# Performance work log

Hardware: AMD Instinct MI355X
Metric: run time of the kernel (lower is better)

The kernel has to match this reference:

```python
import jax, jax.numpy as jnp
import numpy as np

V, D, S, L, H, NC = 32000, 768, 1024, 4, 12, 16
HS = D // H
B = 8

def _layernorm(x, w, b, eps=1e-5):
    mu = jnp.mean(x, axis=-1, keepdims=True)
    var = jnp.mean(jnp.square(x - mu), axis=-1, keepdims=True)
    return (x - mu) * jax.lax.rsqrt(var + eps) * w + b


def setup_inputs() -> dict:
    key = jax.random.key(0)
    ks = jax.random.split(key, 24)
    s = 0.02
    inp = {
        "x": jax.random.randint(ks[0], (B, S), 0, V, dtype=jnp.int64) if jax.config.jax_enable_x64 else jax.random.randint(ks[0], (B, S), 0, V, dtype=jnp.int32),
        "attention_mask": jnp.ones((B, S), dtype=jnp.int32),
        "tok_emb": jax.random.normal(ks[1], (V, D), jnp.float32) * s,
        "pos_emb": jax.random.normal(ks[2], (S, D), jnp.float32) * s,
        "Wq": jax.random.normal(ks[3], (L, H, D, HS), jnp.float32) * s,
        "Wk": jax.random.normal(ks[4], (L, H, D, HS), jnp.float32) * s,
        "Wv": jax.random.normal(ks[5], (L, H, D, HS), jnp.float32) * s,
        "Wo": jax.random.normal(ks[6], (L, D, D), jnp.float32) * s,
        "bo": jnp.zeros((L, D), jnp.float32),
        "ln1_w": jnp.ones((L, D), jnp.float32),
        "ln1_b": jnp.zeros((L, D), jnp.float32),
        "ln2_w": jnp.ones((L, D), jnp.float32),
        "ln2_b": jnp.zeros((L, D), jnp.float32),
        "W1": jax.random.normal(ks[7], (L, D, 4 * D), jnp.float32) * s,
        "b1": jnp.zeros((L, 4 * D), jnp.float32),
        "W2": jax.random.normal(ks[8], (L, 4 * D, D), jnp.float32) * s,
        "b2": jnp.zeros((L, D), jnp.float32),
        "lnf_w": jnp.ones((D,), jnp.float32),
        "lnf_b": jnp.zeros((D,), jnp.float32),
        "cW1": jax.random.normal(ks[9], (D, 4 * D), jnp.float32) * s,
        "cb1": jnp.zeros((4 * D,), jnp.float32),
        "cW2": jax.random.normal(ks[10], (4 * D, NC), jnp.float32) * s,
        "cb2": jnp.zeros((NC,), jnp.float32),
    }
    return inp


def reference(x, attention_mask, tok_emb, pos_emb, Wq, Wk, Wv, Wo, bo,
              ln1_w, ln1_b, ln2_w, ln2_b, W1, b1, W2, b2,
              lnf_w, lnf_b, cW1, cb1, cW2, cb2):
    b, s = x.shape
    h = tok_emb[x] + pos_emb[jnp.arange(s)][None, :, :]  # [B,S,D]
    key_mask = (attention_mask == 0)[:, None, None, :]   # [B,1,1,S] masks keys
    scale = jnp.asarray(D, h.dtype) ** -0.5              # NOTE: scales by embed_dim, as in source
    for l in range(L):
        xn = _layernorm(h, ln1_w[l], ln1_b[l])
        q = jnp.einsum('bsd,hde->bhse', xn, Wq[l])
        k = jnp.einsum('bsd,hde->bhse', xn, Wk[l])
        v = jnp.einsum('bsd,hde->bhse', xn, Wv[l])
        wei = jnp.einsum('bhqe,bhke->bhqk', q, k) * scale
        wei = jnp.where(key_mask, -jnp.inf, wei)
        att = jax.nn.softmax(wei, axis=-1)               # dropout = identity (eval)
        out = jnp.einsum('bhqk,bhke->bhqe', att, v)      # [B,H,S,HS]
        out = out.transpose(0, 2, 1, 3).reshape(b, s, D)  # concat heads
        h = h + out @ Wo[l] + bo[l]
        xn2 = _layernorm(h, ln2_w[l], ln2_b[l])
        h = h + jax.nn.relu(xn2 @ W1[l] + b1[l]) @ W2[l] + b2[l]
    h = _layernorm(h, lnf_w, lnf_b)
    last = h[:, -1, :]                                   # pool=None -> last position
    logits = jax.nn.relu(last @ cW1 + cb1) @ cW2 + cb2
    return logits
```

## Files before the change

kernel.cpp:

```cpp
#include <hip/hip_runtime.h>
#include <hip/hip_bf16.h>

#define D_MODEL 768
#define SEQ     1024
#define NB      8
#define NHEAD   12
#define HS      64
#define NLAYER  4
#define DFF     3072
#define NCLS    16
#define MROWS   (NB*SEQ)

typedef float f32x4  __attribute__((ext_vector_type(4)));
typedef short bf16x8 __attribute__((ext_vector_type(8)));

__device__ __forceinline__ short f2bf_s(float x) {
    __hip_bfloat16 h = __float2bfloat16(x);
    union { __hip_bfloat16 h; short s; } u; u.h = h; return u.s;
}

__device__ __forceinline__ void gld16(const void* g, void* l) {
    __builtin_amdgcn_global_load_lds((const __attribute__((address_space(1))) void*)g,
                                     (__attribute__((address_space(3))) void*)l, 16, 0, 0);
}

__global__ __launch_bounds__(256) void embed_kernel(
    const int* __restrict__ x, const float* __restrict__ tok,
    const float* __restrict__ pos, float* __restrict__ h)
{
    int row = blockIdx.x;
    int s   = row & (SEQ - 1);
    int t   = threadIdx.x;
    int id  = x[row];
    const float* te = tok + (size_t)id * D_MODEL;
    const float* pe = pos + (size_t)s  * D_MODEL;
    float* hr = h + (size_t)row * D_MODEL;
    for (int d = t; d < D_MODEL; d += 256) hr[d] = te[d] + pe[d];
}

template<int BF16OUT>
__global__ __launch_bounds__(256) void ln_kernel(
    const float* __restrict__ in, const float* __restrict__ w,
    const float* __restrict__ b, void* __restrict__ outv,
    int row_stride, int row_offset)
{
    __shared__ float red[256];
    int r = blockIdx.x;
    const float* xr = in + (size_t)(r * row_stride + row_offset) * D_MODEL;
    int t = threadIdx.x;
    float v0 = xr[t], v1 = xr[t + 256], v2 = xr[t + 512];
    red[t] = v0 + v1 + v2; __syncthreads();
    for (int off = 128; off; off >>= 1) { if (t < off) red[t] += red[t + off]; __syncthreads(); }
    float mu = red[0] * (1.f / D_MODEL);
    __syncthreads();
    float d0 = v0 - mu, d1 = v1 - mu, d2 = v2 - mu;
    red[t] = d0*d0 + d1*d1 + d2*d2; __syncthreads();
    for (int off = 128; off; off >>= 1) { if (t < off) red[t] += red[t + off]; __syncthreads(); }
    float rstd = rsqrtf(red[0] * (1.f / D_MODEL) + 1e-5f);
    float y0 = d0 * rstd * w[t]       + b[t];
    float y1 = d1 * rstd * w[t + 256] + b[t + 256];
    float y2 = d2 * rstd * w[t + 512] + b[t + 512];
    if (BF16OUT) {
        __hip_bfloat16* yr = (__hip_bfloat16*)outv + (size_t)r * D_MODEL;
        yr[t] = __float2bfloat16(y0); yr[t+256] = __float2bfloat16(y1); yr[t+512] = __float2bfloat16(y2);
    } else {
        float* yr = (float*)outv + (size_t)r * D_MODEL;
        yr[t] = y0; yr[t+256] = y1; yr[t+512] = y2;
    }
}

template<int MODE>
__global__ __launch_bounds__(256) void convw_kernel(
    const float* __restrict__ W, __hip_bfloat16* __restrict__ BT,
    int K, int N, size_t in_stride, size_t out_stride)
{
    __shared__ __hip_bfloat16 sT[64][72];
    W  += (size_t)blockIdx.z * in_stride;
    BT += (size_t)blockIdx.z * out_stride;
    int k0 = blockIdx.x * 64, n0 = blockIdx.y * 64;
    int t = threadIdx.x;
    int kl = t >> 4, nl4 = (t & 15) * 4;
    #pragma unroll
    for (int i = 0; i < 4; i++) {
        int k = k0 + kl + i * 16;
        int n = n0 + nl4;
        const float* src = (MODE == 0) ? (W + (size_t)k * N + n)
                                       : (W + ((size_t)(n >> 6) * K + k) * 64 + (n & 63));
        float4 v = *(const float4*)src;
        sT[nl4 + 0][kl + i*16] = __float2bfloat16(v.x);
        sT[nl4 + 1][kl + i*16] = __float2bfloat16(v.y);
        sT[nl4 + 2][kl + i*16] = __float2bfloat16(v.z);
        sT[nl4 + 3][kl + i*16] = __float2bfloat16(v.w);
    }
    __syncthreads();
    int nl = t >> 2, seg = (t & 3) * 16;
    uint4* dst = (uint4*)(BT + (size_t)(n0 + nl) * K + k0 + seg);
    dst[0] = *(uint4*)&sT[nl][seg];
    dst[1] = *(uint4*)&sT[nl][seg + 8];
}

template<int OMODE>
__global__ __launch_bounds__(256, 3) void gemm128(
    const __hip_bfloat16* __restrict__ A, const __hip_bfloat16* __restrict__ BT,
    const float* __restrict__ bias, const float* __restrict__ res,
    void* __restrict__ Cv, int M, int N, int K, int relu)
{
    __shared__ short sA[2][128 * 32];
    __shared__ short sB[2][128 * 32];
    int t = threadIdx.x;
    int wave = t >> 6, lane = t & 63;
    int l16 = lane & 15, quad = (lane >> 4) & 3;
    int wm = wave >> 1, wn = wave & 1;
    int bm = blockIdx.x * 128, bn = blockIdx.y * 128;

    int kbeg = 0, kend = K;
    if (OMODE == 3) { int KS = K >> 1; kbeg = blockIdx.z * KS; kend = kbeg + KS; }

    int u = lane >> 2;
    int skey = ((u & 3) ^ ((u >> 2) & 3));
    int sseg = (lane & 3) ^ skey;
    int c0 = wave * 2, c1 = wave * 2 + 1;
    int rA0 = c0 * 16 + u, rA1 = c1 * 16 + u;
    int fkey = ((l16 & 3) ^ ((l16 >> 2) & 3));

    const f32x4 zf = {0.f, 0.f, 0.f, 0.f};
    f32x4 acc[4][4];
    #pragma unroll
    for (int mi = 0; mi < 4; mi++)
        #pragma unroll
        for (int ni = 0; ni < 4; ni++) acc[mi][ni] = zf;

    #define STAGE(bufi, kk) do { \
        gld16(A  + (size_t)(bm + rA0) * K + (kk) + sseg * 8, &sA[bufi][c0 * 512]); \
        gld16(A  + (size_t)(bm + rA1) * K + (kk) + sseg * 8, &sA[bufi][c1 * 512]); \
        gld16(BT + (size_t)(bn + rA0) * K + (kk) + sseg * 8, &sB[bufi][c0 * 512]); \
        gld16(BT + (size_t)(bn + rA1) * K + (kk) + sseg * 8, &sB[bufi][c1 * 512]); \
    } while (0)

    STAGE(0, kbeg);
    __syncthreads();
    int buf = 0;
    for (int k0 = kbeg; k0 < kend; k0 += 32) {
        int kn = k0 + 32;
        if (kn < kend) STAGE(buf ^ 1, kn);
        bf16x8 aF[4], bF[4];
        #pragma unroll
        for (int mi = 0; mi < 4; mi++)
            aF[mi] = *(bf16x8*)&sA[buf][(wm * 64 + mi * 16 + l16) * 32 + ((quad ^ fkey) * 8)];
        #pragma unroll
        for (int ni = 0; ni < 4; ni++)
            bF[ni] = *(bf16x8*)&sB[buf][(wn * 64 + ni * 16 + l16) * 32 + ((quad ^ fkey) * 8)];
        #pragma unroll
        for (int ni = 0; ni < 4; ni++)
            #pragma unroll
            for (int mi = 0; mi < 4; mi++)
                acc[mi][ni] = __builtin_amdgcn_mfma_f32_16x16x32_bf16(aF[mi], bF[ni], acc[mi][ni], 0, 0, 0);
        __syncthreads();
        buf ^= 1;
    }
    #undef STAGE

    #pragma unroll
    for (int mi = 0; mi < 4; mi++) {
        #pragma unroll
        for (int ni = 0; ni < 4; ni++) {
            int row0 = bm + wm * 64 + mi * 16 + quad * 4;
            int col  = bn + wn * 64 + ni * 16 + l16;
            #pragma unroll
            for (int r = 0; r < 4; r++) {
                int row = row0 + r;
                float v = acc[mi][ni][r];
                if (OMODE == 3) {
                    float* C = (float*)Cv;
                    if (blockIdx.z == 0 && bias) v += bias[col];
                    unsafeAtomicAdd(&C[(size_t)row * N + col], v);
                    continue;
                }
                if (OMODE != 1 && bias) v += bias[col];
                if (relu) v = fmaxf(v, 0.f);
                if (OMODE == 0) {
                    float* C = (float*)Cv;
                    if (res) v += res[(size_t)row * N + col];
                    C[(size_t)row * N + col] = v;
                } else if (OMODE == 1) {
                    int which = col / D_MODEL, cc = col % D_MODEL;
                    int bb = row >> 10, ss = row & 1023, hh = cc >> 6, e = cc & 63;
                    ((__hip_bfloat16*)Cv)[(size_t)which * MROWS * D_MODEL +
                        (((size_t)(bb * NHEAD + hh)) * SEQ + ss) * HS + e] = __float2bfloat16(v);
                } else {
                    ((__hip_bfloat16*)Cv)[(size_t)row * N + col] = __float2bfloat16(v);
                }
            }
        }
    }
    (void)M;
}

__global__ __launch_bounds__(256) void vtrans_kernel(
    const __hip_bfloat16* __restrict__ vb, __hip_bfloat16* __restrict__ vt)
{
    __shared__ short tile[64][66];
    int bh = blockIdx.x, st = blockIdx.y;
    const short* src = (const short*)vb + ((size_t)bh * SEQ + st * 64) * HS;
    int t = threadIdx.x;
    #pragma unroll
    for (int i = 0; i < 2; i++) {
        int slot = t + i * 256;
        int row = slot >> 3, seg = slot & 7;
        *(uint4*)&tile[row][seg * 8] = *(const uint4*)(src + row * HS + seg * 8);
    }
    __syncthreads();
    short* dst = (short*)vt + (size_t)bh * HS * SEQ + st * 64;
    #pragma unroll
    for (int i = 0; i < 2; i++) {
        int slot = t + i * 256;
        int e = slot >> 3, seg = slot & 7;
        union { uint4 u; short s[8]; } pk;
        #pragma unroll
        for (int j = 0; j < 8; j++) pk.s[j] = tile[seg * 8 + j][e];
        *(uint4*)(dst + (size_t)e * SEQ + seg * 8) = pk.u;
    }
}

__global__ __launch_bounds__(128, 2) void attn_mfma_kernel(
    const __hip_bfloat16* __restrict__ q, const __hip_bfloat16* __restrict__ k,
    const __hip_bfloat16* __restrict__ v, const int* __restrict__ mask,
    __hip_bfloat16* __restrict__ ao)
{
    __shared__ short sK[2][64 * 64];
    __shared__ short sVT[2][64 * 64];
    __shared__ short sP[2][64 * 64];
    __shared__ float mskf[SEQ];
    int bid = blockIdx.x;
    int xcd = bid & 7, j = bid >> 3;
    int bh  = ((j >> 3) << 3) | xcd;
    int qt8 = j & 7;
    int b = bh / NHEAD, hh = bh % NHEAD;
    int t = threadIdx.x, w = t >> 6, lane = t & 63;
    int l16 = lane & 15, quad = lane >> 4;
    const float scale = 0.036084391824351615f;
    const f32x4 zf = {0.f, 0.f, 0.f, 0.f};

    #pragma unroll
    for (int i = 0; i < 8; i++) {
        int idx = t + i * 128;
        mskf[idx] = mask[b * SEQ + idx] ? 0.f : -1e30f;
    }

    int qb0 = qt8 * 128 + w * 64;
    const __hip_bfloat16* qbase = q + ((size_t)bh * SEQ + qb0) * HS;
    bf16x8 qf[4][2];
    #pragma unroll
    for (int qt = 0; qt < 4; qt++)
        #pragma unroll
        for (int s = 0; s < 2; s++)
            qf[qt][s] = *(const bf16x8*)(qbase + (qt * 16 + l16) * HS + s * 32 + quad * 8);

    f32x4 accO[4][4];
    float m_st[4], l_st[4];
    #pragma unroll
    for (int dt = 0; dt < 4; dt++)
        #pragma unroll
        for (int qt = 0; qt < 4; qt++) accO[dt][qt] = zf;
    #pragma unroll
    for (int qt = 0; qt < 4; qt++) { m_st[qt] = -1e30f; l_st[qt] = 0.f; }

    int rowL = lane >> 3;
    int sgl = ((lane & 7) ^ ((lane >> 3) & 7)) * 8;
    const __hip_bfloat16* kg0 = k + ((size_t)bh * SEQ) * HS;
    const __hip_bfloat16* vtg0 = v + (size_t)bh * HS * SEQ;
    short* myP = &sP[w][0];

    #pragma unroll
    for (int i = 0; i < 4; i++) {
        int c = w * 4 + i;
        int rr = c * 8 + rowL;
        gld16(kg0  + (size_t)rr * HS  + sgl, (char*)&sK[0][0]  + c * 1024);
        gld16(vtg0 + (size_t)rr * SEQ + sgl, (char*)&sVT[0][0] + c * 1024);
    }
    __syncthreads();

    int buf = 0;
    for (int kc = 0; kc < 16; kc++) {
        if (kc < 15) {
            const __hip_bfloat16* kg  = kg0  + (size_t)(kc + 1) * 64 * HS;
            const __hip_bfloat16* vtg = vtg0 + (kc + 1) * 64;
            #pragma unroll
            for (int i = 0; i < 4; i++) {
                int c = w * 4 + i;
                int rr = c * 8 + rowL;
                gld16(kg  + (size_t)rr * HS  + sgl, (char*)&sK[buf ^ 1][0]  + c * 1024);
                gld16(vtg + (size_t)rr * SEQ + sgl, (char*)&sVT[buf ^ 1][0] + c * 1024);
            }
        }
        short* cK  = &sK[buf][0];
        short* cVT = &sVT[buf][0];

        bf16x8 vf[4][2];
        #pragma unroll
        for (int dt = 0; dt < 4; dt++)
            #pragma unroll
            for (int s = 0; s < 2; s++)
                vf[dt][s] = *(bf16x8*)&cVT[(dt * 16 + l16) * 64 + (((s * 4 + quad) ^ (l16 & 7)) * 8)];
        f32x4 sc[4][4];
        #pragma unroll
        for (int kt = 0; kt < 4; kt++) {
            bf16x8 kf0 = *(bf16x8*)&cK[(kt * 16 + l16) * 64 + ((quad ^ (l16 & 7)) * 8)];
            bf16x8 kf1 = *(bf16x8*)&cK[(kt * 16 + l16) * 64 + (((4 + quad) ^ (l16 & 7)) * 8)];
            #pragma unroll
            for (int qt = 0; qt < 4; qt++) {
                f32x4 c = __builtin_amdgcn_mfma_f32_16x16x32_bf16(kf0, qf[qt][0], zf, 0, 0, 0);
                sc[kt][qt] = __builtin_amdgcn_mfma_f32_16x16x32_bf16(kf1, qf[qt][1], c, 0, 0, 0);
            }
        }
        #pragma unroll
        for (int kt = 0; kt < 4; kt++) {
            f32x4 mk = *(f32x4*)&mskf[kc * 64 + kt * 16 + quad * 4];
            #pragma unroll
            for (int qt = 0; qt < 4; qt++)
                #pragma unroll
                for (int r = 0; r < 4; r++)
                    sc[kt][qt][r] = sc[kt][qt][r] * scale + mk[r];
        }
        #pragma unroll
        for (int qt = 0; qt < 4; qt++) {
            float rm = -1e30f;
            #pragma unroll
            for (int kt = 0; kt < 4; kt++)
                #pragma unroll
                for (int r = 0; r < 4; r++) rm = fmaxf(rm, sc[kt][qt][r]);
            rm = fmaxf(rm, __shfl_xor(rm, 16));
            rm = fmaxf(rm, __shfl_xor(rm, 32));
            float mnew = fmaxf(m_st[qt], rm);
            float corr = __expf(m_st[qt] - mnew);
            m_st[qt] = mnew;
            float ps = 0.f;
            #pragma unroll
            for (int kt = 0; kt < 4; kt++) {
                union { uint2 u; short s[4]; } pk;
                #pragma unroll
                for (int r = 0; r < 4; r++) {
                    float p = __expf(sc[kt][qt][r] - mnew);
                    ps += p;
                    pk.s[r] = f2bf_s(p);
                }
                *(uint2*)&myP[(qt * 16 + l16) * 64 +
                              (((kt * 2 + (quad >> 1)) ^ (l16 & 7)) * 8) + (quad & 1) * 4] = pk.u;
            }
            ps += __shfl_xor(ps, 16);
            ps += __shfl_xor(ps, 32);
            l_st[qt] = l_st[qt] * corr + ps;
            #pragma unroll
            for (int dt = 0; dt < 4; dt++) accO[dt][qt] *= corr;
        }
        asm volatile("" ::: "memory");
        #pragma unroll
        for (int qt = 0; qt < 4; qt++) {
            bf16x8 pf0 = *(bf16x8*)&myP[(qt * 16 + l16) * 64 + ((quad ^ (l16 & 7)) * 8)];
            bf16x8 pf1 = *(bf16x8*)&myP[(qt * 16 + l16) * 64 + (((4 + quad) ^ (l16 & 7)) * 8)];
            #pragma unroll
            for (int dt = 0; dt < 4; dt++) {
                accO[dt][qt] = __builtin_amdgcn_mfma_f32_16x16x32_bf16(vf[dt][0], pf0, accO[dt][qt], 0, 0, 0);
                accO[dt][qt] = __builtin_amdgcn_mfma_f32_16x16x32_bf16(vf[dt][1], pf1, accO[dt][qt], 0, 0, 0);
            }
        }
        __syncthreads();
        buf ^= 1;
    }

    #pragma unroll
    for (int qt = 0; qt < 4; qt++) {
        float inv = 1.f / l_st[qt];
        int row = qb0 + qt * 16 + l16;
        __hip_bfloat16* orow = ao + ((size_t)(b * SEQ + row)) * D_MODEL + hh * HS;
        #pragma unroll
        for (int dt = 0; dt < 4; dt++) {
            union { uint2 u; short s[4]; } pk;
            #pragma unroll
            for (int r = 0; r < 4; r++) pk.s[r] = f2bf_s(accO[dt][qt][r] * inv);
            *(uint2*)(orow + dt * 16 + quad * 4) = pk.u;
        }
    }
}

__global__ __launch_bounds__(256) void fc1_kernel(
    const float* __restrict__ A, const float* __restrict__ W,
    const float* __restrict__ bias, float* __restrict__ out)
{
    __shared__ float sa[D_MODEL];
    int row = blockIdx.x, t = threadIdx.x;
    for (int i = t; i < D_MODEL; i += 256) sa[i] = A[(size_t)row * D_MODEL + i];
    __syncthreads();
    int col = blockIdx.y * 256 + t;
    float s = 0.f;
    #pragma unroll 8
    for (int kk = 0; kk < D_MODEL; kk++) s = fmaf(sa[kk], W[(size_t)kk * DFF + col], s);
    s += bias[col];
    out[(size_t)row * DFF + col] = fmaxf(s, 0.f);
}

__global__ __launch_bounds__(256) void fc2_kernel(
    const float* __restrict__ A, const float* __restrict__ W,
    const float* __restrict__ bias, float* __restrict__ out)
{
    __shared__ float wred[4][NCLS];
    int row = blockIdx.x, t = threadIdx.x;
    int wave = t >> 6, lane = t & 63;
    const float* a = A + (size_t)row * DFF;
    float acc[NCLS];
    #pragma unroll
    for (int c = 0; c < NCLS; c++) acc[c] = 0.f;
    for (int kk = t; kk < DFF; kk += 256) {
        float av = a[kk];
        const float4* wr = (const float4*)(W + (size_t)kk * NCLS);
        float4 w0 = wr[0], w1 = wr[1], w2 = wr[2], w3 = wr[3];
        acc[0]  = fmaf(av, w0.x, acc[0]);  acc[1]  = fmaf(av, w0.y, acc[1]);
        acc[2]  = fmaf(av, w0.z, acc[2]);  acc[3]  = fmaf(av, w0.w, acc[3]);
        acc[4]  = fmaf(av, w1.x, acc[4]);  acc[5]  = fmaf(av, w1.y, acc[5]);
        acc[6]  = fmaf(av, w1.z, acc[6]);  acc[7]  = fmaf(av, w1.w, acc[7]);
        acc[8]  = fmaf(av, w2.x, acc[8]);  acc[9]  = fmaf(av, w2.y, acc[9]);
        acc[10] = fmaf(av, w2.z, acc[10]); acc[11] = fmaf(av, w2.w, acc[11]);
        acc[12] = fmaf(av, w3.x, acc[12]); acc[13] = fmaf(av, w3.y, acc[13]);
        acc[14] = fmaf(av, w3.z, acc[14]); acc[15] = fmaf(av, w3.w, acc[15]);
    }
    #pragma unroll
    for (int c = 0; c < NCLS; c++)
        #pragma unroll
        for (int off = 32; off; off >>= 1) acc[c] += __shfl_down(acc[c], off);
    if (lane == 0)
        #pragma unroll
        for (int c = 0; c < NCLS; c++) wred[wave][c] = acc[c];
    __syncthreads();
    if (t < NCLS)
        out[row * NCLS + t] = wred[0][t] + wred[1][t] + wred[2][t] + wred[3][t] + bias[t];
}

extern "C" void kernel_launch(void* const* d_in, const int* in_sizes, int n_in,
                              void* d_out, int out_size, void* d_ws, size_t ws_size,
                              hipStream_t stream)
{
    const int*   x     = (const int*)  d_in[0];
    const int*   amask = (const int*)  d_in[1];
    const float* tok   = (const float*)d_in[2];
    const float* pos   = (const float*)d_in[3];
    const float* Wq    = (const float*)d_in[4];
    const float* Wk    = (const float*)d_in[5];
    const float* Wv    = (const float*)d_in[6];
    const float* Wo    = (const float*)d_in[7];
    const float* bo    = (const float*)d_in[8];
    const float* ln1w  = (const float*)d_in[9];
    const float* ln1b  = (const float*)d_in[10];
    const float* ln2w  = (const float*)d_in[11];
    const float* ln2b  = (const float*)d_in[12];
    const float* W1    = (const float*)d_in[13];
    const float* b1    = (const float*)d_in[14];
    const float* W2    = (const float*)d_in[15];
    const float* b2    = (const float*)d_in[16];
    const float* lnfw  = (const float*)d_in[17];
    const float* lnfb  = (const float*)d_in[18];
    const float* cW1   = (const float*)d_in[19];
    const float* cb1   = (const float*)d_in[20];
    const float* cW2   = (const float*)d_in[21];
    const float* cb2   = (const float*)d_in[22];

    char* base = (char*)d_ws;
    const size_t MD = (size_t)MROWS * D_MODEL;
    float* h = (float*)base;                         base += MD * 4;
    __hip_bfloat16* xn = (__hip_bfloat16*)base;      base += MD * 2;
    __hip_bfloat16* qb = (__hip_bfloat16*)base;      base += MD * 2;
    __hip_bfloat16* kb = (__hip_bfloat16*)base;      base += MD * 2;
    __hip_bfloat16* vb = (__hip_bfloat16*)base;      base += MD * 2;
    __hip_bfloat16* vT = (__hip_bfloat16*)base;      base += MD * 2;
    __hip_bfloat16* ff = (__hip_bfloat16*)base;      base += (size_t)MROWS * DFF * 2;
    float* lnf = (float*)base;                       base += (size_t)NB * D_MODEL * 4;
    float* cls = (float*)base;                       base += (size_t)NB * DFF * 4;
    __hip_bfloat16* wQKV = (__hip_bfloat16*)base;    base += (size_t)NLAYER * 3 * D_MODEL * D_MODEL * 2;
    __hip_bfloat16* wTo = (__hip_bfloat16*)base;     base += (size_t)NLAYER * D_MODEL * D_MODEL * 2;
    __hip_bfloat16* wT1 = (__hip_bfloat16*)base;     base += (size_t)NLAYER * D_MODEL * DFF * 2;
    __hip_bfloat16* wT2 = (__hip_bfloat16*)base;     base += (size_t)NLAYER * DFF * D_MODEL * 2;

    const size_t SQW = (size_t)D_MODEL * D_MODEL;
    const size_t SFF = (size_t)D_MODEL * DFF;

    convw_kernel<1><<<dim3(12,12,4), 256, 0, stream>>>(Wq, wQKV + 0 * SQW, D_MODEL, D_MODEL, SQW, 3 * SQW);
    convw_kernel<1><<<dim3(12,12,4), 256, 0, stream>>>(Wk, wQKV + 1 * SQW, D_MODEL, D_MODEL, SQW, 3 * SQW);
    convw_kernel<1><<<dim3(12,12,4), 256, 0, stream>>>(Wv, wQKV + 2 * SQW, D_MODEL, D_MODEL, SQW, 3 * SQW);
    convw_kernel<0><<<dim3(12,12,4), 256, 0, stream>>>(Wo, wTo, D_MODEL, D_MODEL, SQW, SQW);
    convw_kernel<0><<<dim3(12,48,4), 256, 0, stream>>>(W1, wT1, D_MODEL, DFF, SFF, SFF);
    convw_kernel<0><<<dim3(48,12,4), 256, 0, stream>>>(W2, wT2, DFF, D_MODEL, SFF, SFF);

    embed_kernel<<<MROWS, 256, 0, stream>>>(x, tok, pos, h);

    dim3 gQKV(MROWS / 128, (3 * D_MODEL) / 128);
    dim3 gDS(MROWS / 128, D_MODEL / 128, 2);
    dim3 gF(MROWS / 128, DFF / 128);
    for (int l = 0; l < NLAYER; l++) {
        ln_kernel<1><<<MROWS, 256, 0, stream>>>(h, ln1w + l * D_MODEL, ln1b + l * D_MODEL, xn, 1, 0);
        gemm128<1><<<gQKV, 256, 0, stream>>>(xn, wQKV + l * 3 * SQW, nullptr, nullptr, qb, MROWS, 3 * D_MODEL, D_MODEL, 0);
        vtrans_kernel<<<dim3(NB * NHEAD, SEQ / 64), 256, 0, stream>>>(vb, vT);
        attn_mfma_kernel<<<NB * NHEAD * 8, 128, 0, stream>>>(qb, kb, vT, amask, xn);
        gemm128<3><<<gDS, 256, 0, stream>>>(xn, wTo + l * SQW, bo + l * D_MODEL, nullptr, h, MROWS, D_MODEL, D_MODEL, 0);
        ln_kernel<1><<<MROWS, 256, 0, stream>>>(h, ln2w + l * D_MODEL, ln2b + l * D_MODEL, xn, 1, 0);
        gemm128<2><<<gF, 256, 0, stream>>>(xn, wT1 + l * SFF, b1 + l * DFF, nullptr, ff, MROWS, DFF, D_MODEL, 1);
        gemm128<3><<<gDS, 256, 0, stream>>>(ff, wT2 + l * SFF, b2 + l * D_MODEL, nullptr, h, MROWS, D_MODEL, DFF, 0);
    }
    ln_kernel<0><<<NB, 256, 0, stream>>>(h, lnfw, lnfb, lnf, SEQ, SEQ - 1);
    fc1_kernel<<<dim3(NB, DFF / 256), 256, 0, stream>>>(lnf, cW1, cb1, cls);
    fc2_kernel<<<NB, 256, 0, stream>>>(cls, cW2, cb2, (float*)d_out);
}
```

Before: 1.753 ms.

## Triple-buffer GEMM loads with explicit vmcnt waits and warp-shuffle layernorm reductions

The GEMM main loop moves from double to triple buffering of the LDS tiles. Global-to-LDS loads are issued two steps ahead and guarded by explicit s_waitcnt vmcnt counts and raw s_barriers, and the per-step address arithmetic is replaced by precomputed base pointers. The aim is to hide global memory latency behind the MFMA work, at the cost of extra LDS per block, which may lower occupancy below the launch-bounds target of 3 blocks. Layernorm also switches from a shared-memory tree reduction to wave shuffles with a small partial array, cutting the number of barriers.

```diff
diff --git a/kernel.cpp b/kernel.cpp
--- a/kernel.cpp
+++ b/kernel.cpp
@@ -44,19 +44,24 @@
     const float* __restrict__ b, void* __restrict__ outv,
     int row_stride, int row_offset)
 {
-    __shared__ float red[256];
+    __shared__ float part[8];
     int r = blockIdx.x;
     const float* xr = in + (size_t)(r * row_stride + row_offset) * D_MODEL;
-    int t = threadIdx.x;
+    int t = threadIdx.x, wave = t >> 6, lane = t & 63;
     float v0 = xr[t], v1 = xr[t + 256], v2 = xr[t + 512];
-    red[t] = v0 + v1 + v2; __syncthreads();
-    for (int off = 128; off; off >>= 1) { if (t < off) red[t] += red[t + off]; __syncthreads(); }
-    float mu = red[0] * (1.f / D_MODEL);
-    __syncthreads();
+    float s = v0 + v1 + v2;
+    #pragma unroll
+    for (int off = 32; off; off >>= 1) s += __shfl_xor(s, off);
+    if (lane == 0) part[wave] = s;
+    __syncthreads();
+    float mu = (part[0] + part[1] + part[2] + part[3]) * (1.f / D_MODEL);
     float d0 = v0 - mu, d1 = v1 - mu, d2 = v2 - mu;
-    red[t] = d0*d0 + d1*d1 + d2*d2; __syncthreads();
-    for (int off = 128; off; off >>= 1) { if (t < off) red[t] += red[t + off]; __syncthreads(); }
-    float rstd = rsqrtf(red[0] * (1.f / D_MODEL) + 1e-5f);
+    float q = d0*d0 + d1*d1 + d2*d2;
+    #pragma unroll
+    for (int off = 32; off; off >>= 1) q += __shfl_xor(q, off);
+    if (lane == 0) part[4 + wave] = q;
+    __syncthreads();
+    float rstd = rsqrtf((part[4] + part[5] + part[6] + part[7]) * (1.f / D_MODEL) + 1e-5f);
     float y0 = d0 * rstd * w[t]       + b[t];
     float y1 = d1 * rstd * w[t + 256] + b[t + 256];
     float y2 = d2 * rstd * w[t + 512] + b[t + 512];
@@ -105,8 +110,8 @@
     const float* __restrict__ bias, const float* __restrict__ res,
     void* __restrict__ Cv, int M, int N, int K, int relu)
 {
-    __shared__ short sA[2][128 * 32];
-    __shared__ short sB[2][128 * 32];
+    __shared__ short sA[3][128 * 32];
+    __shared__ short sB[3][128 * 32];
     int t = threadIdx.x;
     int wave = t >> 6, lane = t & 63;
     int l16 = lane & 15, quad = (lane >> 4) & 3;
@@ -115,6 +120,7 @@
 
     int kbeg = 0, kend = K;
     if (OMODE == 3) { int KS = K >> 1; kbeg = blockIdx.z * KS; kend = kbeg + KS; }
+    int nsteps = (kend - kbeg) >> 5;
 
     int u = lane >> 2;
     int skey = ((u & 3) ^ ((u >> 2) & 3));
@@ -130,33 +136,54 @@
         #pragma unroll
         for (int ni = 0; ni < 4; ni++) acc[mi][ni] = zf;
 
+    const __hip_bfloat16* pA0 = A  + (size_t)(bm + rA0) * K + kbeg + sseg * 8;
+    const __hip_bfloat16* pA1 = A  + (size_t)(bm + rA1) * K + kbeg + sseg * 8;
+    const __hip_bfloat16* pB0 = BT + (size_t)(bn + rA0) * K + kbeg + sseg * 8;
+    const __hip_bfloat16* pB1 = BT + (size_t)(bn + rA1) * K + kbeg + sseg * 8;
+
     #define STAGE(bufi, kk) do { \
-        gld16(A  + (size_t)(bm + rA0) * K + (kk) + sseg * 8, &sA[bufi][c0 * 512]); \
-        gld16(A  + (size_t)(bm + rA1) * K + (kk) + sseg * 8, &sA[bufi][c1 * 512]); \
-        gld16(BT + (size_t)(bn + rA0) * K + (kk) + sseg * 8, &sB[bufi][c0 * 512]); \
-        gld16(BT + (size_t)(bn + rA1) * K + (kk) + sseg * 8, &sB[bufi][c1 * 512]); \
+        gld16(pA0 + (kk), &sA[bufi][c0 * 512]); \
+        gld16(pA1 + (kk), &sA[bufi][c1 * 512]); \
+        gld16(pB0 + (kk), &sB[bufi][c0 * 512]); \
+        gld16(pB1 + (kk), &sB[bufi][c1 * 512]); \
     } while (0)
 
-    STAGE(0, kbeg);
-    __syncthreads();
-    int buf = 0;
-    for (int k0 = kbeg; k0 < kend; k0 += 32) {
-        int kn = k0 + 32;
-        if (kn < kend) STAGE(buf ^ 1, kn);
+    STAGE(0, 0);
+    if (nsteps > 1) STAGE(1, 32);
+
+    int bufr = 0, bufs = 2;
+    for (int it = 0; it < nsteps; ++it) {
+        if (it + 1 < nsteps) { asm volatile("s_waitcnt vmcnt(4)" ::: "memory"); }
+        else                 { asm volatile("s_waitcnt vmcnt(0)" ::: "memory"); }
+        __builtin_amdgcn_sched_barrier(0);
+        __builtin_amdgcn_s_barrier();
+        __builtin_amdgcn_sched_barrier(0);
+
+        const short* curA = &sA[bufr][0];
+        const short* curB = &sB[bufr][0];
         bf16x8 aF[4], bF[4];
         #pragma unroll
         for (int mi = 0; mi < 4; mi++)
-            aF[mi] = *(bf16x8*)&sA[buf][(wm * 64 + mi * 16 + l16) * 32 + ((quad ^ fkey) * 8)];
+            aF[mi] = *(const bf16x8*)&curA[(wm * 64 + mi * 16 + l16) * 32 + ((quad ^ fkey) * 8)];
         #pragma unroll
         for (int ni = 0; ni < 4; ni++)
-            bF[ni] = *(bf16x8*)&sB[buf][(wn * 64 + ni * 16 + l16) * 32 + ((quad ^ fkey) * 8)];
+            bF[ni] = *(const bf16x8*)&curB[(wn * 64 + ni * 16 + l16) * 32 + ((quad ^ fkey) * 8)];
+
+        asm volatile("s_waitcnt lgkmcnt(0)" ::: "memory");
+        __builtin_amdgcn_sched_barrier(0);
+        __builtin_amdgcn_s_barrier();
+        __builtin_amdgcn_sched_barrier(0);
+
+        if (it + 2 < nsteps) STAGE(bufs, (it + 2) * 32);
+
         #pragma unroll
         for (int ni = 0; ni < 4; ni++)
             #pragma unroll
             for (int mi = 0; mi < 4; mi++)
                 acc[mi][ni] = __builtin_amdgcn_mfma_f32_16x16x32_bf16(aF[mi], bF[ni], acc[mi][ni], 0, 0, 0);
-        __syncthreads();
-        buf ^= 1;
+
+        bufr = (bufr == 2) ? 0 : bufr + 1;
+        bufs = (bufs == 2) ? 0 : bufs + 1;
     }
     #undef STAGE
 
```

Result: faster. 1.675 ms (-4.5%).
